# Optimization experiments

Hardware: AMD Instinct MI355X
Metric: run time of the kernel (lower is better)

Reference implementation:

```python
import jax, jax.numpy as jnp
import numpy as np

GAMMA = 3.0  # self.gamma; gamma_dic is empty in the source, so gamma == self.gamma for all samples
N, C = 8192, 32000

def setup_inputs() -> dict:
    key = jax.random.key(0)
    k1, k2 = jax.random.split(key)
    inp = jax.random.normal(k1, (N, C), dtype=jnp.float32)
    target = jax.random.randint(k2, (N,), 0, C, dtype=jnp.int64)
    return {"input": inp, "target": target}

def reference(input, target):
    # logpt = log_softmax(input)[i, target[i]]
    logpt = jax.nn.log_softmax(input, axis=1)                      # [N, C]
    logpt = jnp.take_along_axis(logpt, target[:, None], axis=1)[:, 0]  # [N]
    pt = jnp.exp(logpt)
    # gamma_dic in the source is empty, so get_gamma_list yields self.gamma everywhere
    loss = -((1.0 - pt) ** GAMMA) * logpt
    return loss.sum()  # size_average=False -> sum
```

## Files before the change

kernel.cpp:

```cpp
#include <hip/hip_runtime.h>
#include <math.h>

#define NROWS 8192
#define NCOLS 32000
#define NV4   (NCOLS / 4)
#define BLK   256

__global__ __launch_bounds__(BLK) void focal_row_kernel(
    const float* __restrict__ in,
    const int*   __restrict__ tgt,
    float*       __restrict__ row_loss)
{
    const int row = blockIdx.x;
    const int tid = threadIdx.x;
    const float* rp = in + (size_t)row * NCOLS;
    const float4* rp4 = (const float4*)rp;

    float m = -INFINITY;
    float s = 0.0f;
    for (int i = tid; i < NV4; i += BLK) {
        float4 v = rp4[i];
        float vm = fmaxf(fmaxf(v.x, v.y), fmaxf(v.z, v.w));
        float nm = fmaxf(m, vm);
        s = s * __expf(m - nm)
          + __expf(v.x - nm) + __expf(v.y - nm)
          + __expf(v.z - nm) + __expf(v.w - nm);
        m = nm;
    }

    #pragma unroll
    for (int off = 1; off < 64; off <<= 1) {
        float om = __shfl_xor(m, off, 64);
        float os = __shfl_xor(s, off, 64);
        float nm = fmaxf(m, om);
        s = s * __expf(m - nm) + os * __expf(om - nm);
        m = nm;
    }

    __shared__ float sm[4];
    __shared__ float ss[4];
    const int wave = tid >> 6;
    const int lane = tid & 63;
    if (lane == 0) { sm[wave] = m; ss[wave] = s; }
    __syncthreads();

    if (tid == 0) {
        float M = sm[0], S = ss[0];
        #pragma unroll
        for (int w = 1; w < 4; ++w) {
            float nm = fmaxf(M, sm[w]);
            S = S * __expf(M - nm) + ss[w] * __expf(sm[w] - nm);
            M = nm;
        }
        float lse   = M + logf(S);
        float xt    = rp[tgt[row]];
        float logpt = xt - lse;
        float pt    = __expf(logpt);
        float u     = 1.0f - pt;
        row_loss[row] = -(u * u * u) * logpt;
    }
}

__global__ __launch_bounds__(BLK) void sum_kernel(
    const float* __restrict__ row_loss,
    float*       __restrict__ out)
{
    const int tid = threadIdx.x;
    float acc = 0.0f;
    for (int i = tid; i < NROWS; i += BLK) acc += row_loss[i];

    #pragma unroll
    for (int off = 1; off < 64; off <<= 1) acc += __shfl_xor(acc, off, 64);

    __shared__ float ws[4];
    const int wave = tid >> 6;
    const int lane = tid & 63;
    if (lane == 0) ws[wave] = acc;
    __syncthreads();
    if (tid == 0) out[0] = ws[0] + ws[1] + ws[2] + ws[3];
}

extern "C" void kernel_launch(void* const* d_in, const int* in_sizes, int n_in,
                              void* d_out, int out_size, void* d_ws, size_t ws_size,
                              hipStream_t stream) {
    const float* in  = (const float*)d_in[0];
    const int*   tgt = (const int*)d_in[1];
    float* out = (float*)d_out;
    float* ws  = (float*)d_ws;

    focal_row_kernel<<<NROWS, BLK, 0, stream>>>(in, tgt, ws);
    sum_kernel<<<1, BLK, 0, stream>>>(ws, out);
}
```

Measured before the change: 192.1 us.

## Process one row per wave with dual accumulators and atomic final sum

Each 64-lane wave now owns one row instead of a 256-thread block sharing it, which removes the shared-memory and barrier cross-wave reduction per row. The inner loop loads two float4s per iteration into two independent online-softmax accumulators to raise memory-level parallelism, uses nontemporal loads, and only rescales the running sum when the max increases. The separate sum kernel is replaced by a memset plus one atomicAdd per block, which makes the float summation order nondeterministic. The target logit is loaded up front so its latency overlaps the streaming loop.

```diff
diff --git a/kernel.cpp b/kernel.cpp
--- a/kernel.cpp
+++ b/kernel.cpp
@@ -3,30 +3,47 @@
 
 #define NROWS 8192
 #define NCOLS 32000
-#define NV4   (NCOLS / 4)
+#define NV4   8000
 #define BLK   256
+#define ROWS_PER_BLK 4
 
-__global__ __launch_bounds__(BLK) void focal_row_kernel(
+typedef float f32x4 __attribute__((ext_vector_type(4)));
+
+__device__ __forceinline__ void acc4(const f32x4 v, float& m, float& s) {
+    float vm = fmaxf(fmaxf(v.x, v.y), fmaxf(v.z, v.w));
+    if (vm > m) { s *= __expf(m - vm); m = vm; }
+    s += __expf(v.x - m) + __expf(v.y - m) + __expf(v.z - m) + __expf(v.w - m);
+}
+
+__global__ __launch_bounds__(BLK) void focal_wave_kernel(
     const float* __restrict__ in,
     const int*   __restrict__ tgt,
-    float*       __restrict__ row_loss)
+    float*       __restrict__ out)
 {
-    const int row = blockIdx.x;
-    const int tid = threadIdx.x;
-    const float* rp = in + (size_t)row * NCOLS;
-    const float4* rp4 = (const float4*)rp;
+    const int wave = threadIdx.x >> 6;
+    const int lane = threadIdx.x & 63;
+    const int row  = blockIdx.x * ROWS_PER_BLK + wave;
+    const float*  rp  = in + (size_t)row * NCOLS;
+    const f32x4*  rp4 = (const f32x4*)rp;
 
-    float m = -INFINITY;
-    float s = 0.0f;
-    for (int i = tid; i < NV4; i += BLK) {
-        float4 v = rp4[i];
-        float vm = fmaxf(fmaxf(v.x, v.y), fmaxf(v.z, v.w));
-        float nm = fmaxf(m, vm);
-        s = s * __expf(m - nm)
-          + __expf(v.x - nm) + __expf(v.y - nm)
-          + __expf(v.z - nm) + __expf(v.w - nm);
-        m = nm;
+    const float xt = rp[tgt[row]];
+
+    float m0 = -INFINITY, s0 = 0.0f;
+    float m1 = -INFINITY, s1 = 0.0f;
+    int i = lane;
+    for (int k = 0; k < 62; ++k, i += 128) {
+        f32x4 a = __builtin_nontemporal_load(&rp4[i]);
+        f32x4 b = __builtin_nontemporal_load(&rp4[i + 64]);
+        acc4(a, m0, s0);
+        acc4(b, m1, s1);
     }
+    {
+        f32x4 a = __builtin_nontemporal_load(&rp4[i]);
+        acc4(a, m0, s0);
+    }
+
+    float m = fmaxf(m0, m1);
+    float s = s0 * __expf(m0 - m) + s1 * __expf(m1 - m);
 
     #pragma unroll
     for (int off = 1; off < 64; off <<= 1) {
@@ -37,47 +54,18 @@
         m = nm;
     }
 
-    __shared__ float sm[4];
-    __shared__ float ss[4];
-    const int wave = tid >> 6;
-    const int lane = tid & 63;
-    if (lane == 0) { sm[wave] = m; ss[wave] = s; }
-    __syncthreads();
-
-    if (tid == 0) {
-        float M = sm[0], S = ss[0];
-        #pragma unroll
-        for (int w = 1; w < 4; ++w) {
-            float nm = fmaxf(M, sm[w]);
-            S = S * __expf(M - nm) + ss[w] * __expf(sm[w] - nm);
-            M = nm;
-        }
-        float lse   = M + logf(S);
-        float xt    = rp[tgt[row]];
+    __shared__ float part[ROWS_PER_BLK];
+    if (lane == 0) {
+        float lse   = m + logf(s);
         float logpt = xt - lse;
         float pt    = __expf(logpt);
         float u     = 1.0f - pt;
-        row_loss[row] = -(u * u * u) * logpt;
+        part[wave]  = -(u * u * u) * logpt;
     }
-}
-
-__global__ __launch_bounds__(BLK) void sum_kernel(
-    const float* __restrict__ row_loss,
-    float*       __restrict__ out)
-{
-    const int tid = threadIdx.x;
-    float acc = 0.0f;
-    for (int i = tid; i < NROWS; i += BLK) acc += row_loss[i];
-
-    #pragma unroll
-    for (int off = 1; off < 64; off <<= 1) acc += __shfl_xor(acc, off, 64);
-
-    __shared__ float ws[4];
-    const int wave = tid >> 6;
-    const int lane = tid & 63;
-    if (lane == 0) ws[wave] = acc;
     __syncthreads();
-    if (tid == 0) out[0] = ws[0] + ws[1] + ws[2] + ws[3];
+    if (threadIdx.x == 0) {
+        atomicAdd(out, part[0] + part[1] + part[2] + part[3]);
+    }
 }
 
 extern "C" void kernel_launch(void* const* d_in, const int* in_sizes, int n_in,
@@ -86,8 +74,7 @@
     const float* in  = (const float*)d_in[0];
     const int*   tgt = (const int*)d_in[1];
     float* out = (float*)d_out;
-    float* ws  = (float*)d_ws;
 
-    focal_row_kernel<<<NROWS, BLK, 0, stream>>>(in, tgt, ws);
-    sum_kernel<<<1, BLK, 0, stream>>>(ws, out);
+    (void)hipMemsetAsync(out, 0, sizeof(float), stream);
+    focal_wave_kernel<<<NROWS / ROWS_PER_BLK, BLK, 0, stream>>>(in, tgt, out);
 }
```

Result: faster. 172.9 us (-10.0%).
